# Kernel tuning notes

Hardware: AMD Instinct MI355X
Metric: run time of the kernel (lower is better)

## Reference

```python
import jax, jax.numpy as jnp
import numpy as np

EMBED_DIM = 1024
NUM_HEADS = 16
EFF_HEADS = NUM_HEADS // 2
HEAD_DIM = EMBED_DIM // NUM_HEADS
LAMBDA_INIT = 0.8
B, N = 2, 2048


def setup_inputs() -> dict:
    key = jax.random.key(0)
    ks = jax.random.split(key, 14)
    s = 0.02
    return {
        "x": jax.random.normal(ks[0], (B, N, EMBED_DIM), dtype=jnp.float32),
        "Wq": jax.random.normal(ks[1], (EMBED_DIM, EMBED_DIM), dtype=jnp.float32) * s,
        "bq": jnp.zeros((EMBED_DIM,), dtype=jnp.float32),
        "Wk": jax.random.normal(ks[2], (EMBED_DIM, EMBED_DIM), dtype=jnp.float32) * s,
        "bk": jnp.zeros((EMBED_DIM,), dtype=jnp.float32),
        "Wv": jax.random.normal(ks[3], (EMBED_DIM, EMBED_DIM), dtype=jnp.float32) * s,
        "bv": jnp.zeros((EMBED_DIM,), dtype=jnp.float32),
        "Wp": jax.random.normal(ks[4], (EMBED_DIM, EMBED_DIM), dtype=jnp.float32) * s,
        "bp": jnp.zeros((EMBED_DIM,), dtype=jnp.float32),
        "lambda_q1": jax.random.normal(ks[5], (EFF_HEADS, 1, HEAD_DIM), dtype=jnp.float32) * s,
        "lambda_k1": jax.random.normal(ks[6], (EFF_HEADS, 1, HEAD_DIM), dtype=jnp.float32) * s,
        "lambda_q2": jax.random.normal(ks[7], (EFF_HEADS, 1, HEAD_DIM), dtype=jnp.float32) * s,
        "lambda_k2": jax.random.normal(ks[8], (EFF_HEADS, 1, HEAD_DIM), dtype=jnp.float32) * s,
    }


def reference(x, Wq, bq, Wk, bk, Wv, bv, Wp, bp,
              lambda_q1, lambda_k1, lambda_q2, lambda_k2):
    Bb, Nn, C = x.shape
    H, H2, hd = NUM_HEADS, EFF_HEADS, HEAD_DIM
    scale = hd ** (-0.5)

    # projections (torch Linear: y = x @ W.T + b), reshape to [B,H,N,hd]
    q = (x @ Wq.T + bq).reshape(Bb, Nn, H, hd).transpose(0, 2, 1, 3)
    k = (x @ Wk.T + bk).reshape(Bb, Nn, H, hd).transpose(0, 2, 1, 3)
    v = (x @ Wv.T + bv).reshape(Bb, Nn, H, hd).transpose(0, 2, 1, 3)

    q1, q2 = q[:, :H2], q[:, H2:]
    k1, k2 = k[:, :H2], k[:, H2:]
    v1, v2 = v[:, :H2], v[:, H2:]

    # scalar lambda: per-head dot products, clamped exp, differenced, averaged
    l1 = jnp.exp(jnp.minimum((lambda_q1 * lambda_k1).sum((-1, -2)), 5.0))  # [H2]
    l2 = jnp.exp(jnp.minimum((lambda_q2 * lambda_k2).sum((-1, -2)), 5.0))
    lv = (l1 - l2 + LAMBDA_INIT).mean()

    a1 = jax.nn.softmax(jnp.einsum('bhnd,bhmd->bhnm', q1, k1) * scale, axis=-1)
    x1 = jnp.einsum('bhnm,bhmd->bhnd', a1, v1).transpose(0, 2, 1, 3).reshape(Bb, Nn, C // 2)
    a2 = jax.nn.softmax(jnp.einsum('bhnd,bhmd->bhnm', q2, k2) * scale, axis=-1)
    x2 = jnp.einsum('bhnm,bhmd->bhnd', a2, v2).transpose(0, 2, 1, 3).reshape(Bb, Nn, C // 2)

    out = jnp.concatenate([x1 - lv * x2, x2], axis=-1) @ Wp.T + bp
    return out
```

## Files before the change

kernel.cpp:

```cpp
#include <hip/hip_runtime.h>

typedef __bf16 bf16;
typedef __bf16 bf16x8 __attribute__((ext_vector_type(8)));
typedef __bf16 bf16x4 __attribute__((ext_vector_type(4)));
typedef float  f32x16 __attribute__((ext_vector_type(16)));
typedef unsigned int uint;
typedef unsigned int uintx4 __attribute__((ext_vector_type(4)));

#define QSCALE (0.125f * 1.44269504088896340736f)

__device__ __forceinline__ void g2l16(const void* g, void* l) {
  __builtin_amdgcn_global_load_lds(
      (const __attribute__((address_space(1))) void*)g,
      (__attribute__((address_space(3))) void*)l, 16, 0, 0);
}

__device__ __forceinline__ f32x16 mfma16(bf16x8 a, bf16x8 b, f32x16 c) {
  return __builtin_amdgcn_mfma_f32_32x32x16_bf16(a, b, c, 0, 0, 0);
}

__device__ __forceinline__ uint pack_bf16(float a, float b) {
  unsigned short lo = __builtin_bit_cast(unsigned short, (bf16)a);
  unsigned short hi = __builtin_bit_cast(unsigned short, (bf16)b);
  return (uint)lo | ((uint)hi << 16);
}

__global__ void cast5_kernel(const float* __restrict__ x,
                             const float* __restrict__ wq, const float* __restrict__ wk,
                             const float* __restrict__ wv, const float* __restrict__ wp,
                             bf16* __restrict__ xb, bf16* __restrict__ wqkv,
                             bf16* __restrict__ wpb) {
  int seg = blockIdx.y;
  long i = (long)(blockIdx.x * 256 + threadIdx.x) * 8;
  const float* s; bf16* d; long n;
  if (seg == 0)      { s = x;  d = xb;  n = 4194304; }
  else if (seg == 1) { s = wq; d = wqkv;            n = 1048576; }
  else if (seg == 2) { s = wk; d = wqkv + 1048576;  n = 1048576; }
  else if (seg == 3) { s = wv; d = wqkv + 2097152;  n = 1048576; }
  else               { s = wp; d = wpb;             n = 1048576; }
  if (i >= n) return;
  float4 f0 = *(const float4*)(s + i);
  float4 f1 = *(const float4*)(s + i + 4);
  bf16x8 o;
  o[0] = (bf16)f0.x; o[1] = (bf16)f0.y; o[2] = (bf16)f0.z; o[3] = (bf16)f0.w;
  o[4] = (bf16)f1.x; o[5] = (bf16)f1.y; o[6] = (bf16)f1.z; o[7] = (bf16)f1.w;
  *(bf16x8*)(d + i) = o;
}

__global__ void lv_kernel(const float* __restrict__ lq1, const float* __restrict__ lk1,
                          const float* __restrict__ lq2, const float* __restrict__ lk2,
                          float* __restrict__ lvp) {
  int t = threadIdx.x;
  float accum = 0.f;
  for (int hh = 0; hh < 8; ++hh) {
    float v1 = lq1[hh*64 + t] * lk1[hh*64 + t];
    float v2 = lq2[hh*64 + t] * lk2[hh*64 + t];
    for (int off = 32; off; off >>= 1) {
      v1 += __shfl_xor(v1, off);
      v2 += __shfl_xor(v2, off);
    }
    accum += expf(fminf(v1, 5.f)) - expf(fminf(v2, 5.f));
  }
  if (t == 0) *lvp = accum / 8.f + 0.8f;
}

__global__ __launch_bounds__(256, 2) void gemm_qkv_kernel(
    const bf16* __restrict__ A, const bf16* __restrict__ B,
    const float* __restrict__ bias0, const float* __restrict__ bias1,
    const float* __restrict__ bias2,
    bf16* __restrict__ O0, bf16* __restrict__ O1, bf16* __restrict__ O2) {
  __shared__ __align__(16) char smem[32 * 1024];
  const int tid = threadIdx.x;
  const int w = tid >> 6, L = tid & 63;
  const int l31 = L & 31, h5 = L >> 5;
  const int m0 = blockIdx.x * 128;
  const int n0g = blockIdx.y * 128;
  const int by = n0g >> 10;
  const bf16* Bp = B + (long)by * 1048576;
  const float* biasp = (by == 0) ? bias0 : ((by == 1) ? bias1 : bias2);
  const int nloc = n0g & 1023;

  f32x16 acc[2][2];
  for (int i = 0; i < 2; ++i) for (int j = 0; j < 2; ++j)
    for (int r = 0; r < 16; ++r) acc[i][j][r] = 0.f;

  const int srow = L >> 1, spar = L & 1;
  const int wm = w >> 1, wn = w & 1;
  const int fs = (l31 * 2 + h5) * 16;

  for (int k0 = 0; k0 < 1024; k0 += 64) {
    for (int i = 0; i < 8; ++i) {
      int r = w * 8 + i;
      int rr = r & 15;
      int rowblk = rr >> 2, kst = rr & 3;
      int row = rowblk * 32 + srow;
      int kk = k0 + (kst * 2 + spar) * 8;
      const bf16* gsrc = (r < 16) ? (A + (long)(m0 + row) * 1024 + kk)
                                  : (Bp + (long)(nloc + row) * 1024 + kk);
      g2l16(gsrc, smem + r * 1024);
    }
    __syncthreads();
    for (int kst = 0; kst < 4; ++kst) {
      bf16x8 a0 = *(const bf16x8*)(smem + (((wm * 2 + 0) * 4 + kst) * 1024) + fs);
      bf16x8 a1 = *(const bf16x8*)(smem + (((wm * 2 + 1) * 4 + kst) * 1024) + fs);
      bf16x8 b0 = *(const bf16x8*)(smem + 16384 + (((wn * 2 + 0) * 4 + kst) * 1024) + fs);
      bf16x8 b1 = *(const bf16x8*)(smem + 16384 + (((wn * 2 + 1) * 4 + kst) * 1024) + fs);
      acc[0][0] = mfma16(a0, b0, acc[0][0]);
      acc[0][1] = mfma16(a0, b1, acc[0][1]);
      acc[1][0] = mfma16(a1, b0, acc[1][0]);
      acc[1][1] = mfma16(a1, b1, acc[1][1]);
    }
    __syncthreads();
  }

  if (by == 2) {
    int b = m0 >> 11;
    int nbase = (m0 & 2047);
    for (int mi = 0; mi < 2; ++mi) for (int ni = 0; ni < 2; ++ni) {
      int col = nloc + wn * 64 + ni * 32 + l31;
      int hh = col >> 6, d = col & 63;
      float bias_v = biasp[col];
      long rowbase = ((long)(b * 16 + hh) * 64 + d) * 2048
                   + nbase + wm * 64 + mi * 32 + 4 * h5;
      for (int g = 0; g < 4; ++g) {
        bf16x4 pk;
        for (int r = 0; r < 4; ++r) pk[r] = (bf16)(acc[mi][ni][g * 4 + r] + bias_v);
        *(bf16x4*)(O2 + rowbase + 8 * g) = pk;
      }
    }
  } else {
    bf16* dst = (by == 0) ? O0 : O1;
    float scale = (by == 0) ? QSCALE : 1.0f;
    for (int mi = 0; mi < 2; ++mi) for (int ni = 0; ni < 2; ++ni) {
      int col = nloc + wn * 64 + ni * 32 + l31;
      float bias_v = biasp[col];
      int row_base = m0 + wm * 64 + mi * 32 + 4 * h5;
      for (int reg = 0; reg < 16; ++reg) {
        int rowoff = (reg & 3) + 8 * (reg >> 2);
        float v = (acc[mi][ni][reg] + bias_v) * scale;
        dst[(long)(row_base + rowoff) * 1024 + col] = (bf16)v;
      }
    }
  }
}

__global__ __launch_bounds__(256, 2) void gemm_proj_kernel(
    const bf16* __restrict__ A, const bf16* __restrict__ B,
    const float* __restrict__ bias, float* __restrict__ Of) {
  __shared__ __align__(16) char smem[24 * 1024];
  const int tid = threadIdx.x;
  const int w = tid >> 6, L = tid & 63;
  const int l31 = L & 31, h5 = L >> 5;
  const int m0 = blockIdx.x * 64;
  const int nloc = blockIdx.y * 128;

  f32x16 acc[2];
  for (int i = 0; i < 2; ++i)
    for (int r = 0; r < 16; ++r) acc[i][r] = 0.f;

  const int srow = L >> 1, spar = L & 1;
  const int fs = (l31 * 2 + h5) * 16;

  for (int k0 = 0; k0 < 1024; k0 += 64) {
    for (int i = 0; i < 6; ++i) {
      int r = w * 6 + i;
      const bf16* gsrc;
      if (r < 8) {
        int rowblk = r >> 2, kst = r & 3;
        gsrc = A + (long)(m0 + rowblk * 32 + srow) * 1024 + k0 + (kst * 2 + spar) * 8;
      } else {
        int rr = r - 8;
        int rowblk = rr >> 2, kst = rr & 3;
        gsrc = B + (long)(nloc + rowblk * 32 + srow) * 1024 + k0 + (kst * 2 + spar) * 8;
      }
      g2l16(gsrc, smem + r * 1024);
    }
    __syncthreads();
    for (int kst = 0; kst < 4; ++kst) {
      bf16x8 a0 = *(const bf16x8*)(smem + ((0 * 4 + kst) * 1024) + fs);
      bf16x8 a1 = *(const bf16x8*)(smem + ((1 * 4 + kst) * 1024) + fs);
      bf16x8 bb = *(const bf16x8*)(smem + 8192 + ((w * 4 + kst) * 1024) + fs);
      acc[0] = mfma16(a0, bb, acc[0]);
      acc[1] = mfma16(a1, bb, acc[1]);
    }
    __syncthreads();
  }

  for (int mi = 0; mi < 2; ++mi) {
    int col = nloc + w * 32 + l31;
    float bias_v = bias[col];
    int row_base = m0 + mi * 32 + 4 * h5;
    for (int reg = 0; reg < 16; ++reg) {
      int rowoff = (reg & 3) + 8 * (reg >> 2);
      Of[(long)(row_base + rowoff) * 1024 + col] = acc[mi][reg] + bias_v;
    }
  }
}

__global__ __launch_bounds__(512, 4) void attn_kernel(
    const bf16* __restrict__ Qb, const bf16* __restrict__ Kb,
    const bf16* __restrict__ Vt, bf16* __restrict__ Ob) {
  __shared__ __align__(16) char smem[34816];
  const int tid = threadIdx.x, w = tid >> 6, L = tid & 63;
  const int half = w >> 2, pair = w & 3;
  const int bh = blockIdx.x, qt = blockIdx.y;
  const int b = bh >> 4, h = bh & 15;
  const int q0 = qt * 128 + pair * 32;
  const int l31 = L & 31, h5 = L >> 5;
  const int srow = L >> 1, spar = L & 1;
  const int fs = (l31 * 2 + h5) * 16;
  char* kbase = smem + half * 16384;

  bf16x8 qf[4];
  for (int kst = 0; kst < 4; ++kst)
    qf[kst] = *(const bf16x8*)(Qb + (long)(b * 2048 + q0 + l31) * 1024 + h * 64
                               + kst * 16 + h5 * 8);

  f32x16 o[2];
  for (int i = 0; i < 2; ++i)
    for (int r = 0; r < 16; ++r) o[i][r] = 0.f;
  float lsum = 0.f;

  const bf16* Kbh = Kb + (long)b * 2048 * 1024 + h * 64 + (long)half * 1024 * 1024;
  const bf16* Vth = Vt + (long)bh * 64 * 2048 + half * 1024;

  for (int t = 0; t < 16; ++t) {
    int n0 = t * 64;
    for (int i = 0; i < 4; ++i) {
      int r = pair * 4 + i;
      if (r < 8) {
        int nkb = r >> 2, kst = r & 3;
        const bf16* g = Kbh + (long)(n0 + nkb * 32 + srow) * 1024 + (kst * 2 + spar) * 8;
        g2l16(g, kbase + r * 1024);
      } else {
        int rr = r - 8, db = rr >> 2, kst = rr & 3;
        const bf16* g = Vth + (long)(db * 32 + srow) * 2048 + n0 + (kst * 2 + spar) * 8;
        g2l16(g, kbase + 8192 + rr * 1024);
      }
    }
    __syncthreads();

    f32x16 s[2];
    for (int i = 0; i < 2; ++i)
      for (int r = 0; r < 16; ++r) s[i][r] = 0.f;
    for (int kst = 0; kst < 4; ++kst) {
      bf16x8 k0f = *(const bf16x8*)(kbase + ((0 * 4 + kst) * 1024) + fs);
      bf16x8 k1f = *(const bf16x8*)(kbase + ((4 + kst) * 1024) + fs);
      s[0] = mfma16(k0f, qf[kst], s[0]);
      s[1] = mfma16(k1f, qf[kst], s[1]);
    }

    for (int nki = 0; nki < 2; ++nki)
      for (int r = 0; r < 16; ++r) {
        float p = __builtin_amdgcn_exp2f(s[nki][r]);
        s[nki][r] = p;
        lsum += p;
      }

    for (int kst = 0; kst < 4; ++kst) {
      bf16x8 v0 = *(const bf16x8*)(kbase + 8192 + ((0 * 4 + kst) * 1024) + fs);
      bf16x8 v1 = *(const bf16x8*)(kbase + 8192 + ((4 + kst) * 1024) + fs);
      int nki = kst >> 1;
      int rbase = (kst & 1) * 8;
      uint p0a = pack_bf16(s[nki][rbase + 0], s[nki][rbase + 1]);
      uint p0b = pack_bf16(s[nki][rbase + 2], s[nki][rbase + 3]);
      uint p1a = pack_bf16(s[nki][rbase + 4], s[nki][rbase + 5]);
      uint p1b = pack_bf16(s[nki][rbase + 6], s[nki][rbase + 7]);
      uint t0 = h5 ? p0a : p1a;
      uint t1 = h5 ? p0b : p1b;
      uint r0 = (uint)__shfl_xor((int)t0, 32);
      uint r1 = (uint)__shfl_xor((int)t1, 32);
      uintx4 uv;
      uv.x = h5 ? r0 : p0a;
      uv.y = h5 ? r1 : p0b;
      uv.z = h5 ? p1a : r0;
      uv.w = h5 ? p1b : r1;
      bf16x8 pf = __builtin_bit_cast(bf16x8, uv);
      o[0] = mfma16(v0, pf, o[0]);
      o[1] = mfma16(v1, pf, o[1]);
    }
    __syncthreads();
  }

  float lcol = lsum + __shfl_xor(lsum, 32);
  if (half) {
    float* dstO = (float*)smem + pair * 2112;
    for (int di = 0; di < 2; ++di)
      for (int r = 0; r < 16; ++r) dstO[L * 33 + di * 16 + r] = o[di][r];
    if (h5 == 0) ((float*)(smem + 33792))[pair * 32 + l31] = lcol;
  }
  __syncthreads();
  float linv = 0.f;
  if (!half) {
    float* srcO = (float*)smem + pair * 2112;
    for (int di = 0; di < 2; ++di)
      for (int r = 0; r < 16; ++r) o[di][r] += srcO[L * 33 + di * 16 + r];
    float lother = ((float*)(smem + 33792))[pair * 32 + l31];
    linv = 1.f / (lcol + lother);
  }
  __syncthreads();
  if (!half) {
    char* ot = smem + pair * 4352;
    for (int di = 0; di < 2; ++di)
      for (int g = 0; g < 4; ++g) {
        bf16x4 pk;
        for (int r = 0; r < 4; ++r)
          pk[r] = (bf16)(o[di][g * 4 + r] * linv);
        int d0 = di * 32 + g * 8 + h5 * 4;
        *(bf16x4*)(ot + (l31 * 68 + d0) * 2) = pk;
      }
    for (int i = 0; i < 4; ++i) {
      int qloc = (L >> 3) + i * 8;
      int cc = L & 7;
      bf16x8 vv = *(const bf16x8*)(ot + (qloc * 68 + cc * 8) * 2);
      *(bf16x8*)(Ob + (long)(b * 2048 + q0 + qloc) * 1024 + h * 64 + cc * 8) = vv;
    }
  }
}

__global__ void combine_kernel(bf16* __restrict__ Ob, const float* __restrict__ lvp) {
  float lv = *lvp;
  int idx = blockIdx.x * 256 + threadIdx.x;
  int row = idx >> 6;
  int j = (idx & 63) * 8;
  bf16x8 o1 = *(const bf16x8*)(Ob + (long)row * 1024 + j);
  bf16x8 o2 = *(const bf16x8*)(Ob + (long)row * 1024 + 512 + j);
  bf16x8 c1;
  for (int e = 0; e < 8; ++e) c1[e] = (bf16)((float)o1[e] - lv * (float)o2[e]);
  *(bf16x8*)(Ob + (long)row * 1024 + j) = c1;
}

extern "C" void kernel_launch(void* const* d_in, const int* in_sizes, int n_in,
                              void* d_out, int out_size, void* d_ws, size_t ws_size,
                              hipStream_t stream) {
  const float* x   = (const float*)d_in[0];
  const float* Wq  = (const float*)d_in[1];
  const float* bq  = (const float*)d_in[2];
  const float* Wk  = (const float*)d_in[3];
  const float* bk  = (const float*)d_in[4];
  const float* Wv  = (const float*)d_in[5];
  const float* bv  = (const float*)d_in[6];
  const float* Wp  = (const float*)d_in[7];
  const float* bp  = (const float*)d_in[8];
  const float* lq1 = (const float*)d_in[9];
  const float* lk1 = (const float*)d_in[10];
  const float* lq2 = (const float*)d_in[11];
  const float* lk2 = (const float*)d_in[12];
  float* out = (float*)d_out;

  char* ws = (char*)d_ws;
  float* lvp = (float*)ws;
  bf16* xb   = (bf16*)(ws + 1024);
  bf16* Wqkv = xb + (long)4096 * 1024;
  bf16* Wpb  = Wqkv + (long)3 * 1024 * 1024;
  bf16* Vt   = Wpb + (long)1024 * 1024;
  bf16* Ob   = Vt + (long)4096 * 1024;
  bf16* Qb = (bf16*)d_out;
  bf16* Kb = Qb + (long)4096 * 1024;

  cast5_kernel<<<dim3(2048, 5), 256, 0, stream>>>(x, Wq, Wk, Wv, Wp, xb, Wqkv, Wpb);
  lv_kernel<<<1, 64, 0, stream>>>(lq1, lk1, lq2, lk2, lvp);
  gemm_qkv_kernel<<<dim3(32, 24), 256, 0, stream>>>(
      xb, Wqkv, bq, bk, bv, Qb, Kb, Vt);
  attn_kernel<<<dim3(32, 16), 512, 0, stream>>>(Qb, Kb, Vt, Ob);
  combine_kernel<<<1024, 256, 0, stream>>>(Ob, lvp);
  gemm_proj_kernel<<<dim3(64, 8), 256, 0, stream>>>(Ob, Wpb, bp, out);
}
```

Baseline: 210.0 us.

## Fold lambda combine into projection weights, widen proj K tile, split softmax sums

Removes the lv and combine kernels. The lambda subtraction is folded algebraically into the bf16 cast of Wp: the right half of each Wp row gets W2 - lv*W1, so the projection consumes the raw concatenated attention outputs. The projection GEMM doubles its K step to 128 with 48KB of LDS, halving barriers per K loop. The attention row-sum now uses four independent accumulators to break the dependency chain. The risk is that every thread of the Wp cast blocks recomputes lambda redundantly, and the different bf16 rounding on folded weights may shift accuracy.

Result: no change. 213.0 us (+1.5%).

```diff
diff --git a/kernel.cpp b/kernel.cpp
--- a/kernel.cpp
+++ b/kernel.cpp
@@ -28,6 +28,8 @@
 __global__ void cast5_kernel(const float* __restrict__ x,
                              const float* __restrict__ wq, const float* __restrict__ wk,
                              const float* __restrict__ wv, const float* __restrict__ wp,
+                             const float* __restrict__ lq1, const float* __restrict__ lk1,
+                             const float* __restrict__ lq2, const float* __restrict__ lk2,
                              bf16* __restrict__ xb, bf16* __restrict__ wqkv,
                              bf16* __restrict__ wpb) {
   int seg = blockIdx.y;
@@ -41,27 +43,28 @@
   if (i >= n) return;
   float4 f0 = *(const float4*)(s + i);
   float4 f1 = *(const float4*)(s + i + 4);
+  if (seg == 4 && (i & 1023) >= 512) {
+    int t = threadIdx.x & 63;
+    float accum = 0.f;
+    for (int hh = 0; hh < 8; ++hh) {
+      float v1 = lq1[hh*64 + t] * lk1[hh*64 + t];
+      float v2 = lq2[hh*64 + t] * lk2[hh*64 + t];
+      for (int off = 32; off; off >>= 1) {
+        v1 += __shfl_xor(v1, off);
+        v2 += __shfl_xor(v2, off);
+      }
+      accum += expf(fminf(v1, 5.f)) - expf(fminf(v2, 5.f));
+    }
+    float lv = accum / 8.f + 0.8f;
+    float4 g0 = *(const float4*)(s + i - 512);
+    float4 g1 = *(const float4*)(s + i - 508);
+    f0.x -= lv * g0.x; f0.y -= lv * g0.y; f0.z -= lv * g0.z; f0.w -= lv * g0.w;
+    f1.x -= lv * g1.x; f1.y -= lv * g1.y; f1.z -= lv * g1.z; f1.w -= lv * g1.w;
+  }
   bf16x8 o;
   o[0] = (bf16)f0.x; o[1] = (bf16)f0.y; o[2] = (bf16)f0.z; o[3] = (bf16)f0.w;
   o[4] = (bf16)f1.x; o[5] = (bf16)f1.y; o[6] = (bf16)f1.z; o[7] = (bf16)f1.w;
   *(bf16x8*)(d + i) = o;
-}
-
-__global__ void lv_kernel(const float* __restrict__ lq1, const float* __restrict__ lk1,
-                          const float* __restrict__ lq2, const float* __restrict__ lk2,
-                          float* __restrict__ lvp) {
-  int t = threadIdx.x;
-  float accum = 0.f;
-  for (int hh = 0; hh < 8; ++hh) {
-    float v1 = lq1[hh*64 + t] * lk1[hh*64 + t];
-    float v2 = lq2[hh*64 + t] * lk2[hh*64 + t];
-    for (int off = 32; off; off >>= 1) {
-      v1 += __shfl_xor(v1, off);
-      v2 += __shfl_xor(v2, off);
-    }
-    accum += expf(fminf(v1, 5.f)) - expf(fminf(v2, 5.f));
-  }
-  if (t == 0) *lvp = accum / 8.f + 0.8f;
 }
 
 __global__ __launch_bounds__(256, 2) void gemm_qkv_kernel(
@@ -147,7 +150,7 @@
 __global__ __launch_bounds__(256, 2) void gemm_proj_kernel(
     const bf16* __restrict__ A, const bf16* __restrict__ B,
     const float* __restrict__ bias, float* __restrict__ Of) {
-  __shared__ __align__(16) char smem[24 * 1024];
+  __shared__ __align__(16) char smem[48 * 1024];
   const int tid = threadIdx.x;
   const int w = tid >> 6, L = tid & 63;
   const int l31 = L & 31, h5 = L >> 5;
@@ -161,25 +164,25 @@
   const int srow = L >> 1, spar = L & 1;
   const int fs = (l31 * 2 + h5) * 16;
 
-  for (int k0 = 0; k0 < 1024; k0 += 64) {
-    for (int i = 0; i < 6; ++i) {
-      int r = w * 6 + i;
+  for (int k0 = 0; k0 < 1024; k0 += 128) {
+    for (int i = 0; i < 12; ++i) {
+      int r = w * 12 + i;
       const bf16* gsrc;
-      if (r < 8) {
-        int rowblk = r >> 2, kst = r & 3;
+      if (r < 16) {
+        int rowblk = r >> 3, kst = r & 7;
         gsrc = A + (long)(m0 + rowblk * 32 + srow) * 1024 + k0 + (kst * 2 + spar) * 8;
       } else {
-        int rr = r - 8;
-        int rowblk = rr >> 2, kst = rr & 3;
+        int rr = r - 16;
+        int rowblk = rr >> 3, kst = rr & 7;
         gsrc = B + (long)(nloc + rowblk * 32 + srow) * 1024 + k0 + (kst * 2 + spar) * 8;
       }
       g2l16(gsrc, smem + r * 1024);
     }
     __syncthreads();
-    for (int kst = 0; kst < 4; ++kst) {
-      bf16x8 a0 = *(const bf16x8*)(smem + ((0 * 4 + kst) * 1024) + fs);
-      bf16x8 a1 = *(const bf16x8*)(smem + ((1 * 4 + kst) * 1024) + fs);
-      bf16x8 bb = *(const bf16x8*)(smem + 8192 + ((w * 4 + kst) * 1024) + fs);
+    for (int kst = 0; kst < 8; ++kst) {
+      bf16x8 a0 = *(const bf16x8*)(smem + ((0 * 8 + kst) * 1024) + fs);
+      bf16x8 a1 = *(const bf16x8*)(smem + ((1 * 8 + kst) * 1024) + fs);
+      bf16x8 bb = *(const bf16x8*)(smem + 16384 + ((w * 8 + kst) * 1024) + fs);
       acc[0] = mfma16(a0, bb, acc[0]);
       acc[1] = mfma16(a1, bb, acc[1]);
     }
@@ -219,7 +222,7 @@
   f32x16 o[2];
   for (int i = 0; i < 2; ++i)
     for (int r = 0; r < 16; ++r) o[i][r] = 0.f;
-  float lsum = 0.f;
+  float ls[4] = {0.f, 0.f, 0.f, 0.f};
 
   const bf16* Kbh = Kb + (long)b * 2048 * 1024 + h * 64 + (long)half * 1024 * 1024;
   const bf16* Vth = Vt + (long)bh * 64 * 2048 + half * 1024;
@@ -254,7 +257,7 @@
       for (int r = 0; r < 16; ++r) {
         float p = __builtin_amdgcn_exp2f(s[nki][r]);
         s[nki][r] = p;
-        lsum += p;
+        ls[r & 3] += p;
       }
 
     for (int kst = 0; kst < 4; ++kst) {
@@ -282,6 +285,7 @@
     __syncthreads();
   }
 
+  float lsum = (ls[0] + ls[1]) + (ls[2] + ls[3]);
   float lcol = lsum + __shfl_xor(lsum, 32);
   if (half) {
     float* dstO = (float*)smem + pair * 2112;
@@ -316,18 +320,6 @@
       *(bf16x8*)(Ob + (long)(b * 2048 + q0 + qloc) * 1024 + h * 64 + cc * 8) = vv;
     }
   }
-}
-
-__global__ void combine_kernel(bf16* __restrict__ Ob, const float* __restrict__ lvp) {
-  float lv = *lvp;
-  int idx = blockIdx.x * 256 + threadIdx.x;
-  int row = idx >> 6;
-  int j = (idx & 63) * 8;
-  bf16x8 o1 = *(const bf16x8*)(Ob + (long)row * 1024 + j);
-  bf16x8 o2 = *(const bf16x8*)(Ob + (long)row * 1024 + 512 + j);
-  bf16x8 c1;
-  for (int e = 0; e < 8; ++e) c1[e] = (bf16)((float)o1[e] - lv * (float)o2[e]);
-  *(bf16x8*)(Ob + (long)row * 1024 + j) = c1;
 }
 
 extern "C" void kernel_launch(void* const* d_in, const int* in_sizes, int n_in,
@@ -349,7 +341,6 @@
   float* out = (float*)d_out;
 
   char* ws = (char*)d_ws;
-  float* lvp = (float*)ws;
   bf16* xb   = (bf16*)(ws + 1024);
   bf16* Wqkv = xb + (long)4096 * 1024;
   bf16* Wpb  = Wqkv + (long)3 * 1024 * 1024;
@@ -358,11 +349,10 @@
   bf16* Qb = (bf16*)d_out;
   bf16* Kb = Qb + (long)4096 * 1024;
 
-  cast5_kernel<<<dim3(2048, 5), 256, 0, stream>>>(x, Wq, Wk, Wv, Wp, xb, Wqkv, Wpb);
-  lv_kernel<<<1, 64, 0, stream>>>(lq1, lk1, lq2, lk2, lvp);
+  cast5_kernel<<<dim3(2048, 5), 256, 0, stream>>>(
+      x, Wq, Wk, Wv, Wp, lq1, lk1, lq2, lk2, xb, Wqkv, Wpb);
   gemm_qkv_kernel<<<dim3(32, 24), 256, 0, stream>>>(
       xb, Wqkv, bq, bk, bv, Qb, Kb, Vt);
   attn_kernel<<<dim3(32, 16), 512, 0, stream>>>(Qb, Kb, Vt, Ob);
-  combine_kernel<<<1024, 256, 0, stream>>>(Ob, lvp);
   gemm_proj_kernel<<<dim3(64, 8), 256, 0, stream>>>(Ob, Wpb, bp, out);
 }
```
